# Optimization experiments

Hardware: AMD Instinct MI355X
Metric: run time of the kernel (lower is better)

## Reference

```python
import jax, jax.numpy as jnp
import numpy as np

H = 32  # hidden_size from LSTMConfig

def setup_inputs() -> dict:
    key = jax.random.key(0)
    ks = jax.random.split(key, 7)
    B, T, F = 131072, 22, 12
    s = 1.0 / np.sqrt(H)
    return {
        "x": jax.random.normal(ks[0], (B, T, F), dtype=jnp.float32),
        "W_ih": jax.random.uniform(ks[1], (4 * H, F), minval=-s, maxval=s, dtype=jnp.float32),
        "W_hh": jax.random.uniform(ks[2], (4 * H, H), minval=-s, maxval=s, dtype=jnp.float32),
        "b_ih": jax.random.uniform(ks[3], (4 * H,), minval=-s, maxval=s, dtype=jnp.float32),
        "b_hh": jax.random.uniform(ks[4], (4 * H,), minval=-s, maxval=s, dtype=jnp.float32),
        "W_head": jax.random.uniform(ks[5], (1, H), minval=-s, maxval=s, dtype=jnp.float32),
        "b_head": jax.random.uniform(ks[6], (1,), minval=-s, maxval=s, dtype=jnp.float32),
    }

def _lstm_last_hidden(x, W_ih, W_hh, b_ih, b_hh):
    B, T, F = x.shape
    # precompute input contribution for all timesteps: [T, B, 4H]
    gx = jnp.einsum('btf,gf->tbg', x, W_ih) + (b_ih + b_hh)

    def step(carry, gx_t):
        h, c = carry
        g = gx_t + h @ W_hh.T                      # [B, 4H]
        i, f, gg, o = jnp.split(g, 4, axis=-1)     # PyTorch gate order i,f,g,o
        i = jax.nn.sigmoid(i)
        f = jax.nn.sigmoid(f)
        gg = jnp.tanh(gg)
        o = jax.nn.sigmoid(o)
        c = f * c + i * gg
        h = o * jnp.tanh(c)
        return (h, c), None

    h0 = jnp.zeros((B, H), dtype=x.dtype)
    (h, _), _ = jax.lax.scan(step, (h0, h0), gx)
    return h  # [B, H] last timestep hidden

def reference(x, W_ih, W_hh, b_ih, b_hh, W_head, b_head):
    h = _lstm_last_hidden(x, W_ih, W_hh, b_ih, b_hh)
    # Dropout p=0.0 is identity; Linear(H,1) + Softplus, then squeeze(-1)
    y = h @ W_head.T + b_head                      # [B, 1]
    return jax.nn.softplus(y)[:, 0]                # [B]
```

## Files before the change

### kernel.cpp

```cpp
#include <hip/hip_runtime.h>
#include <math.h>

#define T_STEPS 22
#define F_IN    12
#define HID     32

typedef __attribute__((ext_vector_type(8))) short  bf16x8;
typedef __attribute__((ext_vector_type(16))) float f32x16;

union FragU { unsigned int u[4]; bf16x8 v; };

#define LOG2E    1.442695041f
#define TWOLOG2E 2.885390082f

static __device__ __forceinline__ unsigned short f2bf(float x) {
    unsigned int u = __builtin_bit_cast(unsigned int, x);
    return (unsigned short)((u + 0x7fffu + ((u >> 16) & 1u)) >> 16);
}

static __device__ __forceinline__ unsigned cvt_pk_bf16(float lo, float hi) {
    unsigned r;
    asm("v_cvt_pk_bf16_f32 %0, %1, %2" : "=v"(r) : "v"(lo), "v"(hi));
    return r;
}

__global__ void prep_kernel(const float* __restrict__ Wih, const float* __restrict__ Whh,
                            const float* __restrict__ bih, const float* __restrict__ bhh,
                            const float* __restrict__ Whead, float* __restrict__ ws) {
    const int tid = threadIdx.x;
    unsigned short* wx = (unsigned short*)ws;
    unsigned short* wh = (unsigned short*)(ws + 1024);
    float* whd = ws + 3072;

    {
        int m = tid >> 6, lane = tid & 63;
        int g = 32 * m + (lane & 31);
        float scale = (m == 2) ? TWOLOG2E : -LOG2E;
        int kbase = 8 * (lane >> 5);
        for (int j = 0; j < 8; ++j) {
            int k = kbase + j;
            float v = 0.0f;
            if (k < F_IN)       v = Wih[g * F_IN + k];
            else if (k == F_IN) v = bih[g] + bhh[g];
            wx[tid * 8 + j] = f2bf(scale * v);
        }
    }
    for (int e = tid; e < 4 * 2 * 64; e += 256) {
        int m = e >> 7, kt = (e >> 6) & 1, lane = e & 63;
        int g = 32 * m + (lane & 31);
        float scale = (m == 2) ? TWOLOG2E : -LOG2E;
        int kbase = 16 * kt + 8 * (lane >> 5);
        for (int j = 0; j < 8; ++j)
            wh[e * 8 + j] = f2bf(scale * Whh[g * HID + kbase + j]);
    }
    if (tid < 32) {
        int hi = tid >> 4, q = tid & 15;
        int j = (q & 3) + 8 * (q >> 2) + 4 * hi;
        whd[tid] = Whead[j];
    }
}

__global__ void __launch_bounds__(256, 2)
lstm_kernel(const float* __restrict__ x, const float* __restrict__ ws,
            const float* __restrict__ bheadp, float* __restrict__ out, int B) {
    const int lane = threadIdx.x & 63;
    const int wave = threadIdx.x >> 6;
    const int col  = lane & 31;
    const int hi   = lane >> 5;
    int b = blockIdx.x * 128 + wave * 32 + col;
    const bool valid = (b < B);
    if (b >= B) b = B - 1;

    const bf16x8* wxp = (const bf16x8*)ws;
    const bf16x8* whp = (const bf16x8*)(ws + 1024);
    bf16x8 wxf[4], whf[4][2];
#pragma unroll
    for (int m = 0; m < 4; ++m) wxf[m] = wxp[m * 64 + lane];
#pragma unroll
    for (int m = 0; m < 4; ++m)
#pragma unroll
        for (int kt = 0; kt < 2; ++kt) whf[m][kt] = whp[(m * 2 + kt) * 64 + lane];

    const float* xb1 = x + (size_t)b * (T_STEPS * F_IN) + (hi ? 8 : 0);
    const float* xb2 = x + (size_t)b * (T_STEPS * F_IN) + (hi ? 8 : 4);

    float c[16], hv[16];
#pragma unroll
    for (int q = 0; q < 16; ++q) { c[q] = 0.0f; hv[q] = 0.0f; }
    bf16x8 hf0, hf1;
#pragma unroll
    for (int j = 0; j < 8; ++j) { hf0[j] = 0; hf1[j] = 0; }

    for (int t = 0; t < T_STEPS; ++t) {
        float4 va = *(const float4*)(xb1 + t * F_IN);
        float4 vb = *(const float4*)(xb2 + t * F_IN);

        FragU xf;
        xf.u[0] = cvt_pk_bf16(va.x, va.y);
        xf.u[1] = cvt_pk_bf16(va.z, va.w);
        unsigned w2 = cvt_pk_bf16(vb.x, vb.y);
        unsigned w3 = cvt_pk_bf16(vb.z, vb.w);
        xf.u[2] = hi ? 0x00003f80u : w2;
        xf.u[3] = hi ? 0u : w3;

        f32x16 a0, a1, a2, a3;
#pragma unroll
        for (int q = 0; q < 16; ++q) { a0[q] = 0.f; a1[q] = 0.f; a2[q] = 0.f; a3[q] = 0.f; }

        a0 = __builtin_amdgcn_mfma_f32_32x32x16_bf16(wxf[0], xf.v, a0, 0, 0, 0);
        a1 = __builtin_amdgcn_mfma_f32_32x32x16_bf16(wxf[1], xf.v, a1, 0, 0, 0);
        a2 = __builtin_amdgcn_mfma_f32_32x32x16_bf16(wxf[2], xf.v, a2, 0, 0, 0);
        a3 = __builtin_amdgcn_mfma_f32_32x32x16_bf16(wxf[3], xf.v, a3, 0, 0, 0);
        a0 = __builtin_amdgcn_mfma_f32_32x32x16_bf16(whf[0][0], hf0, a0, 0, 0, 0);
        a1 = __builtin_amdgcn_mfma_f32_32x32x16_bf16(whf[1][0], hf0, a1, 0, 0, 0);
        a2 = __builtin_amdgcn_mfma_f32_32x32x16_bf16(whf[2][0], hf0, a2, 0, 0, 0);
        a3 = __builtin_amdgcn_mfma_f32_32x32x16_bf16(whf[3][0], hf0, a3, 0, 0, 0);
        a0 = __builtin_amdgcn_mfma_f32_32x32x16_bf16(whf[0][1], hf1, a0, 0, 0, 0);
        a1 = __builtin_amdgcn_mfma_f32_32x32x16_bf16(whf[1][1], hf1, a1, 0, 0, 0);
        a2 = __builtin_amdgcn_mfma_f32_32x32x16_bf16(whf[2][1], hf1, a2, 0, 0, 0);
        a3 = __builtin_amdgcn_mfma_f32_32x32x16_bf16(whf[3][1], hf1, a3, 0, 0, 0);

#pragma unroll
        for (int q = 0; q < 16; ++q) {
            float ri = __builtin_amdgcn_rcpf(1.0f + __builtin_amdgcn_exp2f(a0[q]));
            float rf = __builtin_amdgcn_rcpf(1.0f + __builtin_amdgcn_exp2f(a1[q]));
            float rg = __builtin_amdgcn_rcpf(1.0f + __builtin_amdgcn_exp2f(a2[q]));
            float ro = __builtin_amdgcn_rcpf(1.0f + __builtin_amdgcn_exp2f(a3[q]));
            float gs = fmaf(-2.0f * TWOLOG2E, rg, TWOLOG2E);
            c[q] = fmaf(rf, c[q], ri * gs);
            float tc = fmaf(-2.0f, __builtin_amdgcn_rcpf(1.0f + __builtin_amdgcn_exp2f(c[q])), 1.0f);
            hv[q] = ro * tc;
        }

        unsigned P0 = cvt_pk_bf16(hv[0],  hv[1]);
        unsigned P1 = cvt_pk_bf16(hv[2],  hv[3]);
        unsigned P2 = cvt_pk_bf16(hv[4],  hv[5]);
        unsigned P3 = cvt_pk_bf16(hv[6],  hv[7]);
        unsigned P4 = cvt_pk_bf16(hv[8],  hv[9]);
        unsigned P5 = cvt_pk_bf16(hv[10], hv[11]);
        unsigned P6 = cvt_pk_bf16(hv[12], hv[13]);
        unsigned P7 = cvt_pk_bf16(hv[14], hv[15]);
        asm("v_permlane32_swap_b32 %0, %1" : "+v"(P0), "+v"(P2));
        asm("v_permlane32_swap_b32 %0, %1" : "+v"(P1), "+v"(P3));
        asm("v_permlane32_swap_b32 %0, %1" : "+v"(P4), "+v"(P6));
        asm("v_permlane32_swap_b32 %0, %1" : "+v"(P5), "+v"(P7));
        FragU h0; h0.u[0] = P0; h0.u[1] = P1; h0.u[2] = P2; h0.u[3] = P3;
        FragU h1; h1.u[0] = P4; h1.u[1] = P5; h1.u[2] = P6; h1.u[3] = P7;
        hf0 = h0.v;
        hf1 = h1.v;
    }

    const float* whd = ws + 3072 + hi * 16;
    float y = 0.0f;
#pragma unroll
    for (int q = 0; q < 16; ++q) y = fmaf(hv[q], whd[q], y);
    y += __shfl_xor(y, 32, 64);
    y += bheadp[0];
    float sp = fmaxf(y, 0.0f) + log1pf(expf(-fabsf(y)));
    if (valid && hi == 0) out[b] = sp;
}

extern "C" void kernel_launch(void* const* d_in, const int* in_sizes, int n_in,
                              void* d_out, int out_size, void* d_ws, size_t ws_size,
                              hipStream_t stream) {
    const float* x     = (const float*)d_in[0];
    const float* Wih   = (const float*)d_in[1];
    const float* Whh   = (const float*)d_in[2];
    const float* bih   = (const float*)d_in[3];
    const float* bhh   = (const float*)d_in[4];
    const float* Whead = (const float*)d_in[5];
    const float* bhead = (const float*)d_in[6];
    float* out = (float*)d_out;
    float* ws  = (float*)d_ws;

    const int B = in_sizes[0] / (T_STEPS * F_IN);
    const int blocks = (B + 127) / 128;

    hipLaunchKernelGGL(prep_kernel, dim3(1), dim3(256), 0, stream,
                       Wih, Whh, bih, bhh, Whead, ws);
    hipLaunchKernelGGL(lstm_kernel, dim3(blocks), dim3(256), 0, stream,
                       x, ws, bhead, out, B);
}
```

Baseline: 96.32 us.

## Stage LSTM weight fragments in LDS and cut register pressure in recurrence

```diff
diff --git a/kernel.cpp b/kernel.cpp
--- a/kernel.cpp
+++ b/kernel.cpp
@@ -22,6 +22,10 @@
     unsigned r;
     asm("v_cvt_pk_bf16_f32 %0, %1, %2" : "=v"(r) : "v"(lo), "v"(hi));
     return r;
+}
+
+static __device__ __forceinline__ float bf2f(short s) {
+    return __builtin_bit_cast(float, ((unsigned)(unsigned short)s) << 16);
 }
 
 __global__ void prep_kernel(const float* __restrict__ Wih, const float* __restrict__ Whh,
@@ -54,47 +58,49 @@
             wh[e * 8 + j] = f2bf(scale * Whh[g * HID + kbase + j]);
     }
     if (tid < 32) {
-        int hi = tid >> 4, q = tid & 15;
-        int j = (q & 3) + 8 * (q >> 2) + 4 * hi;
-        whd[tid] = Whead[j];
+        int h2 = tid >> 4, j = tid & 15;
+        int k = (j < 8) ? (8 * h2 + j) : (16 + 8 * h2 + (j - 8));
+        whd[tid] = Whead[k];
     }
 }
 
 __global__ void __launch_bounds__(256, 2)
 lstm_kernel(const float* __restrict__ x, const float* __restrict__ ws,
             const float* __restrict__ bheadp, float* __restrict__ out, int B) {
-    const int lane = threadIdx.x & 63;
-    const int wave = threadIdx.x >> 6;
+    const int tid  = threadIdx.x;
+    const int lane = tid & 63;
+    const int wave = tid >> 6;
     const int col  = lane & 31;
     const int hi   = lane >> 5;
     int b = blockIdx.x * 128 + wave * 32 + col;
     const bool valid = (b < B);
     if (b >= B) b = B - 1;
 
-    const bf16x8* wxp = (const bf16x8*)ws;
-    const bf16x8* whp = (const bf16x8*)(ws + 1024);
-    bf16x8 wxf[4], whf[4][2];
-#pragma unroll
-    for (int m = 0; m < 4; ++m) wxf[m] = wxp[m * 64 + lane];
-#pragma unroll
-    for (int m = 0; m < 4; ++m)
-#pragma unroll
-        for (int kt = 0; kt < 2; ++kt) whf[m][kt] = whp[(m * 2 + kt) * 64 + lane];
+    __shared__ float wlds[3072];
+#pragma unroll
+    for (int i = 0; i < 3; ++i)
+        ((float4*)wlds)[tid + i * 256] = ((const float4*)ws)[tid + i * 256];
+    __syncthreads();
+
+    const bf16x8* wx_l = (const bf16x8*)wlds;
+    const bf16x8* wh_l = ((const bf16x8*)wlds) + 256;
 
     const float* xb1 = x + (size_t)b * (T_STEPS * F_IN) + (hi ? 8 : 0);
     const float* xb2 = x + (size_t)b * (T_STEPS * F_IN) + (hi ? 8 : 4);
 
-    float c[16], hv[16];
-#pragma unroll
-    for (int q = 0; q < 16; ++q) { c[q] = 0.0f; hv[q] = 0.0f; }
+    float c[16];
+#pragma unroll
+    for (int q = 0; q < 16; ++q) c[q] = 0.0f;
     bf16x8 hf0, hf1;
 #pragma unroll
     for (int j = 0; j < 8; ++j) { hf0[j] = 0; hf1[j] = 0; }
 
+#pragma unroll 1
     for (int t = 0; t < T_STEPS; ++t) {
+        asm volatile("" ::: "memory");
+
         float4 va = *(const float4*)(xb1 + t * F_IN);
         float4 vb = *(const float4*)(xb2 + t * F_IN);
-
         FragU xf;
         xf.u[0] = cvt_pk_bf16(va.x, va.y);
         xf.u[1] = cvt_pk_bf16(va.z, va.w);
@@ -107,45 +113,56 @@
 #pragma unroll
         for (int q = 0; q < 16; ++q) { a0[q] = 0.f; a1[q] = 0.f; a2[q] = 0.f; a3[q] = 0.f; }
 
-        a0 = __builtin_amdgcn_mfma_f32_32x32x16_bf16(wxf[0], xf.v, a0, 0, 0, 0);
-        a1 = __builtin_amdgcn_mfma_f32_32x32x16_bf16(wxf[1], xf.v, a1, 0, 0, 0);
-        a2 = __builtin_amdgcn_mfma_f32_32x32x16_bf16(wxf[2], xf.v, a2, 0, 0, 0);
-        a3 = __builtin_amdgcn_mfma_f32_32x32x16_bf16(wxf[3], xf.v, a3, 0, 0, 0);
-        a0 = __builtin_amdgcn_mfma_f32_32x32x16_bf16(whf[0][0], hf0, a0, 0, 0, 0);
-        a1 = __builtin_amdgcn_mfma_f32_32x32x16_bf16(whf[1][0], hf0, a1, 0, 0, 0);
-        a2 = __builtin_amdgcn_mfma_f32_32x32x16_bf16(whf[2][0], hf0, a2, 0, 0, 0);
-        a3 = __builtin_amdgcn_mfma_f32_32x32x16_bf16(whf[3][0], hf0, a3, 0, 0, 0);
-        a0 = __builtin_amdgcn_mfma_f32_32x32x16_bf16(whf[0][1], hf1, a0, 0, 0, 0);
-        a1 = __builtin_amdgcn_mfma_f32_32x32x16_bf16(whf[1][1], hf1, a1, 0, 0, 0);
-        a2 = __builtin_amdgcn_mfma_f32_32x32x16_bf16(whf[2][1], hf1, a2, 0, 0, 0);
-        a3 = __builtin_amdgcn_mfma_f32_32x32x16_bf16(whf[3][1], hf1, a3, 0, 0, 0);
-
-#pragma unroll
-        for (int q = 0; q < 16; ++q) {
-            float ri = __builtin_amdgcn_rcpf(1.0f + __builtin_amdgcn_exp2f(a0[q]));
-            float rf = __builtin_amdgcn_rcpf(1.0f + __builtin_amdgcn_exp2f(a1[q]));
-            float rg = __builtin_amdgcn_rcpf(1.0f + __builtin_amdgcn_exp2f(a2[q]));
-            float ro = __builtin_amdgcn_rcpf(1.0f + __builtin_amdgcn_exp2f(a3[q]));
-            float gs = fmaf(-2.0f * TWOLOG2E, rg, TWOLOG2E);
-            c[q] = fmaf(rf, c[q], ri * gs);
-            float tc = fmaf(-2.0f, __builtin_amdgcn_rcpf(1.0f + __builtin_amdgcn_exp2f(c[q])), 1.0f);
-            hv[q] = ro * tc;
+        a0 = __builtin_amdgcn_mfma_f32_32x32x16_bf16(wx_l[0 * 64 + lane], xf.v, a0, 0, 0, 0);
+        a1 = __builtin_amdgcn_mfma_f32_32x32x16_bf16(wx_l[1 * 64 + lane], xf.v, a1, 0, 0, 0);
+        a2 = __builtin_amdgcn_mfma_f32_32x32x16_bf16(wx_l[2 * 64 + lane], xf.v, a2, 0, 0, 0);
+        a3 = __builtin_amdgcn_mfma_f32_32x32x16_bf16(wx_l[3 * 64 + lane], xf.v, a3, 0, 0, 0);
+        a0 = __builtin_amdgcn_mfma_f32_32x32x16_bf16(wh_l[(0 * 2 + 0) * 64 + lane], hf0, a0, 0, 0, 0);
+        a1 = __builtin_amdgcn_mfma_f32_32x32x16_bf16(wh_l[(1 * 2 + 0) * 64 + lane], hf0, a1, 0, 0, 0);
+        a2 = __builtin_amdgcn_mfma_f32_32x32x16_bf16(wh_l[(2 * 2 + 0) * 64 + lane], hf0, a2, 0, 0, 0);
+        a3 = __builtin_amdgcn_mfma_f32_32x32x16_bf16(wh_l[(3 * 2 + 0) * 64 + lane], hf0, a3, 0, 0, 0);
+        a0 = __builtin_amdgcn_mfma_f32_32x32x16_bf16(wh_l[(0 * 2 + 1) * 64 + lane], hf1, a0, 0, 0, 0);
+        a1 = __builtin_amdgcn_mfma_f32_32x32x16_bf16(wh_l[(1 * 2 + 1) * 64 + lane], hf1, a1, 0, 0, 0);
+        a2 = __builtin_amdgcn_mfma_f32_32x32x16_bf16(wh_l[(2 * 2 + 1) * 64 + lane], hf1, a2, 0, 0, 0);
+        a3 = __builtin_amdgcn_mfma_f32_32x32x16_bf16(wh_l[(3 * 2 + 1) * 64 + lane], hf1, a3, 0, 0, 0);
+        __builtin_amdgcn_sched_group_barrier(0x100, 4, 0);
+        __builtin_amdgcn_sched_group_barrier(0x008, 4, 0);
+        __builtin_amdgcn_sched_group_barrier(0x100, 4, 0);
+        __builtin_amdgcn_sched_group_barrier(0x008, 4, 0);
+        __builtin_amdgcn_sched_group_barrier(0x100, 4, 0);
+        __builtin_amdgcn_sched_group_barrier(0x008, 4, 0);
+
+        unsigned P[8];
+#pragma unroll
+        for (int p = 0; p < 8; ++p) {
+            const int q0 = 2 * p, q1 = 2 * p + 1;
+            float ri0 = __builtin_amdgcn_rcpf(1.0f + __builtin_amdgcn_exp2f(a0[q0]));
+            float rf0 = __builtin_amdgcn_rcpf(1.0f + __builtin_amdgcn_exp2f(a1[q0]));
+            float rg0 = __builtin_amdgcn_rcpf(1.0f + __builtin_amdgcn_exp2f(a2[q0]));
+            float ro0 = __builtin_amdgcn_rcpf(1.0f + __builtin_amdgcn_exp2f(a3[q0]));
+            float gs0 = fmaf(-2.0f * TWOLOG2E, rg0, TWOLOG2E);
+            c[q0] = fmaf(rf0, c[q0], ri0 * gs0);
+            float tc0 = fmaf(-2.0f, __builtin_amdgcn_rcpf(1.0f + __builtin_amdgcn_exp2f(c[q0])), 1.0f);
+            float hv0 = ro0 * tc0;
+
+            float ri1 = __builtin_amdgcn_rcpf(1.0f + __builtin_amdgcn_exp2f(a0[q1]));
+            float rf1 = __builtin_amdgcn_rcpf(1.0f + __builtin_amdgcn_exp2f(a1[q1]));
+            float rg1 = __builtin_amdgcn_rcpf(1.0f + __builtin_amdgcn_exp2f(a2[q1]));
+            float ro1 = __builtin_amdgcn_rcpf(1.0f + __builtin_amdgcn_exp2f(a3[q1]));
+            float gs1 = fmaf(-2.0f * TWOLOG2E, rg1, TWOLOG2E);
+            c[q1] = fmaf(rf1, c[q1], ri1 * gs1);
+            float tc1 = fmaf(-2.0f, __builtin_amdgcn_rcpf(1.0f + __builtin_amdgcn_exp2f(c[q1])), 1.0f);
+            float hv1 = ro1 * tc1;
+
+            P[p] = cvt_pk_bf16(hv0, hv1);
         }
 
-        unsigned P0 = cvt_pk_bf16(hv[0],  hv[1]);
-        unsigned P1 = cvt_pk_bf16(hv[2],  hv[3]);
-        unsigned P2 = cvt_pk_bf16(hv[4],  hv[5]);
-        unsigned P3 = cvt_pk_bf16(hv[6],  hv[7]);
-        unsigned P4 = cvt_pk_bf16(hv[8],  hv[9]);
-        unsigned P5 = cvt_pk_bf16(hv[10], hv[11]);
-        unsigned P6 = cvt_pk_bf16(hv[12], hv[13]);
-        unsigned P7 = cvt_pk_bf16(hv[14], hv[15]);
-        asm("v_permlane32_swap_b32 %0, %1" : "+v"(P0), "+v"(P2));
-        asm("v_permlane32_swap_b32 %0, %1" : "+v"(P1), "+v"(P3));
-        asm("v_permlane32_swap_b32 %0, %1" : "+v"(P4), "+v"(P6));
-        asm("v_permlane32_swap_b32 %0, %1" : "+v"(P5), "+v"(P7));
-        FragU h0; h0.u[0] = P0; h0.u[1] = P1; h0.u[2] = P2; h0.u[3] = P3;
-        FragU h1; h1.u[0] = P4; h1.u[1] = P5; h1.u[2] = P6; h1.u[3] = P7;
+        asm("v_permlane32_swap_b32 %0, %1" : "+v"(P[0]), "+v"(P[2]));
+        asm("v_permlane32_swap_b32 %0, %1" : "+v"(P[1]), "+v"(P[3]));
+        asm("v_permlane32_swap_b32 %0, %1" : "+v"(P[4]), "+v"(P[6]));
+        asm("v_permlane32_swap_b32 %0, %1" : "+v"(P[5]), "+v"(P[7]));
+        FragU h0; h0.u[0] = P[0]; h0.u[1] = P[1]; h0.u[2] = P[2]; h0.u[3] = P[3];
+        FragU h1; h1.u[0] = P[4]; h1.u[1] = P[5]; h1.u[2] = P[6]; h1.u[3] = P[7];
         hf0 = h0.v;
         hf1 = h1.v;
     }
@@ -153,7 +170,10 @@
     const float* whd = ws + 3072 + hi * 16;
     float y = 0.0f;
 #pragma unroll
-    for (int q = 0; q < 16; ++q) y = fmaf(hv[q], whd[q], y);
+    for (int j = 0; j < 8; ++j) {
+        y = fmaf(bf2f(hf0[j]), whd[j], y);
+        y = fmaf(bf2f(hf1[j]), whd[8 + j], y);
+    }
     y += __shfl_xor(y, 32, 64);
     y += bheadp[0];
     float sp = fmaxf(y, 0.0f) + log1pf(expf(-fabsf(y)));
```

Measured after the change: 97.43 us. Within noise of the previous version (+1.2%).

## Switch LSTM recurrence to 16x16x32 MFMA tiles with LDS-resident weights

Applied to the files above, without the earlier changes.

```diff
diff --git a/kernel.cpp b/kernel.cpp
--- a/kernel.cpp
+++ b/kernel.cpp
@@ -6,7 +6,7 @@
 #define HID     32
 
 typedef __attribute__((ext_vector_type(8))) short  bf16x8;
-typedef __attribute__((ext_vector_type(16))) float f32x16;
+typedef __attribute__((ext_vector_type(4)))  float f32x4;
 
 union FragU { unsigned int u[4]; bf16x8 v; };
 
@@ -29,135 +29,156 @@
                             const float* __restrict__ Whead, float* __restrict__ ws) {
     const int tid = threadIdx.x;
     unsigned short* wx = (unsigned short*)ws;
-    unsigned short* wh = (unsigned short*)(ws + 1024);
-    float* whd = ws + 3072;
-
-    {
-        int m = tid >> 6, lane = tid & 63;
-        int g = 32 * m + (lane & 31);
-        float scale = (m == 2) ? TWOLOG2E : -LOG2E;
-        int kbase = 8 * (lane >> 5);
+    unsigned short* wh = (unsigned short*)(ws + 2048);
+    float* whd = ws + 4096;
+
+    for (int e = tid; e < 512; e += 256) {
+        int tile = e >> 6, lane = e & 63;
+        int row = lane & 15, s = lane >> 4;
+        int g = 16 * tile + row;
+        float scale = (tile == 4 || tile == 5) ? TWOLOG2E : -LOG2E;
         for (int j = 0; j < 8; ++j) {
-            int k = kbase + j;
+            int k = 8 * s + j;
             float v = 0.0f;
             if (k < F_IN)       v = Wih[g * F_IN + k];
             else if (k == F_IN) v = bih[g] + bhh[g];
-            wx[tid * 8 + j] = f2bf(scale * v);
+            wx[e * 8 + j] = f2bf(scale * v);
+            int cc = (j < 4) ? (4 * s + j) : (16 + 4 * s + (j - 4));
+            wh[e * 8 + j] = f2bf(scale * Whh[g * HID + cc]);
         }
     }
-    for (int e = tid; e < 4 * 2 * 64; e += 256) {
-        int m = e >> 7, kt = (e >> 6) & 1, lane = e & 63;
-        int g = 32 * m + (lane & 31);
-        float scale = (m == 2) ? TWOLOG2E : -LOG2E;
-        int kbase = 16 * kt + 8 * (lane >> 5);
-        for (int j = 0; j < 8; ++j)
-            wh[e * 8 + j] = f2bf(scale * Whh[g * HID + kbase + j]);
-    }
     if (tid < 32) {
-        int hi = tid >> 4, q = tid & 15;
-        int j = (q & 3) + 8 * (q >> 2) + 4 * hi;
-        whd[tid] = Whead[j];
+        int s = tid >> 3, j = tid & 7;
+        int orig = (j < 4) ? (4 * s + j) : (16 + 4 * s + (j - 4));
+        whd[tid] = Whead[orig];
     }
 }
 
 __global__ void __launch_bounds__(256, 2)
 lstm_kernel(const float* __restrict__ x, const float* __restrict__ ws,
             const float* __restrict__ bheadp, float* __restrict__ out, int B) {
-    const int lane = threadIdx.x & 63;
-    const int wave = threadIdx.x >> 6;
-    const int col  = lane & 31;
-    const int hi   = lane >> 5;
-    int b = blockIdx.x * 128 + wave * 32 + col;
+    const int tid  = threadIdx.x;
+    const int lane = tid & 63;
+    const int wave = tid >> 6;
+    const int col  = lane & 15;
+    const int s    = lane >> 4;
+    int b = blockIdx.x * 64 + wave * 16 + col;
     const bool valid = (b < B);
     if (b >= B) b = B - 1;
 
-    const bf16x8* wxp = (const bf16x8*)ws;
-    const bf16x8* whp = (const bf16x8*)(ws + 1024);
-    bf16x8 wxf[4], whf[4][2];
-#pragma unroll
-    for (int m = 0; m < 4; ++m) wxf[m] = wxp[m * 64 + lane];
-#pragma unroll
-    for (int m = 0; m < 4; ++m)
-#pragma unroll
-        for (int kt = 0; kt < 2; ++kt) whf[m][kt] = whp[(m * 2 + kt) * 64 + lane];
-
-    const float* xb1 = x + (size_t)b * (T_STEPS * F_IN) + (hi ? 8 : 0);
-    const float* xb2 = x + (size_t)b * (T_STEPS * F_IN) + (hi ? 8 : 4);
-
-    float c[16], hv[16];
-#pragma unroll
-    for (int q = 0; q < 16; ++q) { c[q] = 0.0f; hv[q] = 0.0f; }
-    bf16x8 hf0, hf1;
-#pragma unroll
-    for (int j = 0; j < 8; ++j) { hf0[j] = 0; hf1[j] = 0; }
-
+    __shared__ float wlds[4096];
+#pragma unroll
+    for (int i = 0; i < 4; ++i)
+        ((float4*)wlds)[tid + i * 256] = ((const float4*)ws)[tid + i * 256];
+    __syncthreads();
+
+    const bf16x8* wx_l = (const bf16x8*)wlds;
+    const bf16x8* wh_l = ((const bf16x8*)wlds) + 512;
+
+    const float* xr  = x + (size_t)b * (T_STEPS * F_IN);
+    const float* xa  = xr + ((s == 0) ? 0 : 8);
+    const float* xbp = xr + ((s == 0) ? 4 : 8);
+
+    float c0[4], c1[4], h0[4], h1[4];
+#pragma unroll
+    for (int q = 0; q < 4; ++q) { c0[q] = 0.f; c1[q] = 0.f; h0[q] = 0.f; h1[q] = 0.f; }
+    bf16x8 hf;
+#pragma unroll
+    for (int j = 0; j < 8; ++j) hf[j] = 0;
+
+    f32x4 zc;
+#pragma unroll
+    for (int q = 0; q < 4; ++q) zc[q] = 0.0f;
+
+#pragma unroll 1
     for (int t = 0; t < T_STEPS; ++t) {
-        float4 va = *(const float4*)(xb1 + t * F_IN);
-        float4 vb = *(const float4*)(xb2 + t * F_IN);
-
+        asm volatile("" ::: "memory");
+
+        float4 va = *(const float4*)(xa  + t * F_IN);
+        float4 vb = *(const float4*)(xbp + t * F_IN);
+        unsigned p0 = cvt_pk_bf16(va.x, va.y);
+        unsigned p1 = cvt_pk_bf16(va.z, va.w);
+        unsigned p2 = cvt_pk_bf16(vb.x, vb.y);
+        unsigned p3 = cvt_pk_bf16(vb.z, vb.w);
         FragU xf;
-        xf.u[0] = cvt_pk_bf16(va.x, va.y);
-        xf.u[1] = cvt_pk_bf16(va.z, va.w);
-        unsigned w2 = cvt_pk_bf16(vb.x, vb.y);
-        unsigned w3 = cvt_pk_bf16(vb.z, vb.w);
-        xf.u[2] = hi ? 0x00003f80u : w2;
-        xf.u[3] = hi ? 0u : w3;
-
-        f32x16 a0, a1, a2, a3;
-#pragma unroll
-        for (int q = 0; q < 16; ++q) { a0[q] = 0.f; a1[q] = 0.f; a2[q] = 0.f; a3[q] = 0.f; }
-
-        a0 = __builtin_amdgcn_mfma_f32_32x32x16_bf16(wxf[0], xf.v, a0, 0, 0, 0);
-        a1 = __builtin_amdgcn_mfma_f32_32x32x16_bf16(wxf[1], xf.v, a1, 0, 0, 0);
-        a2 = __builtin_amdgcn_mfma_f32_32x32x16_bf16(wxf[2], xf.v, a2, 0, 0, 0);
-        a3 = __builtin_amdgcn_mfma_f32_32x32x16_bf16(wxf[3], xf.v, a3, 0, 0, 0);
-        a0 = __builtin_amdgcn_mfma_f32_32x32x16_bf16(whf[0][0], hf0, a0, 0, 0, 0);
-        a1 = __builtin_amdgcn_mfma_f32_32x32x16_bf16(whf[1][0], hf0, a1, 0, 0, 0);
-        a2 = __builtin_amdgcn_mfma_f32_32x32x16_bf16(whf[2][0], hf0, a2, 0, 0, 0);
-        a3 = __builtin_amdgcn_mfma_f32_32x32x16_bf16(whf[3][0], hf0, a3, 0, 0, 0);
-        a0 = __builtin_amdgcn_mfma_f32_32x32x16_bf16(whf[0][1], hf1, a0, 0, 0, 0);
-        a1 = __builtin_amdgcn_mfma_f32_32x32x16_bf16(whf[1][1], hf1, a1, 0, 0, 0);
-        a2 = __builtin_amdgcn_mfma_f32_32x32x16_bf16(whf[2][1], hf1, a2, 0, 0, 0);
-        a3 = __builtin_amdgcn_mfma_f32_32x32x16_bf16(whf[3][1], hf1, a3, 0, 0, 0);
-
-#pragma unroll
-        for (int q = 0; q < 16; ++q) {
+        if (s == 0)      { xf.u[0] = p0; xf.u[1] = p1; xf.u[2] = p2;          xf.u[3] = p3; }
+        else if (s == 1) { xf.u[0] = p0; xf.u[1] = p1; xf.u[2] = 0x00003f80u; xf.u[3] = 0;  }
+        else             { xf.u[0] = 0;  xf.u[1] = 0;  xf.u[2] = 0;           xf.u[3] = 0;  }
+
+        f32x4 a0, a1, a2, a3, a4, a5, a6, a7;
+        a0 = __builtin_amdgcn_mfma_f32_16x16x32_bf16(wx_l[0 * 64 + lane], xf.v, zc, 0, 0, 0);
+        a1 = __builtin_amdgcn_mfma_f32_16x16x32_bf16(wx_l[1 * 64 + lane], xf.v, zc, 0, 0, 0);
+        a2 = __builtin_amdgcn_mfma_f32_16x16x32_bf16(wx_l[2 * 64 + lane], xf.v, zc, 0, 0, 0);
+        a3 = __builtin_amdgcn_mfma_f32_16x16x32_bf16(wx_l[3 * 64 + lane], xf.v, zc, 0, 0, 0);
+        a4 = __builtin_amdgcn_mfma_f32_16x16x32_bf16(wx_l[4 * 64 + lane], xf.v, zc, 0, 0, 0);
+        a5 = __builtin_amdgcn_mfma_f32_16x16x32_bf16(wx_l[5 * 64 + lane], xf.v, zc, 0, 0, 0);
+        a6 = __builtin_amdgcn_mfma_f32_16x16x32_bf16(wx_l[6 * 64 + lane], xf.v, zc, 0, 0, 0);
+        a7 = __builtin_amdgcn_mfma_f32_16x16x32_bf16(wx_l[7 * 64 + lane], xf.v, zc, 0, 0, 0);
+        a0 = __builtin_amdgcn_mfma_f32_16x16x32_bf16(wh_l[0 * 64 + lane], hf, a0, 0, 0, 0);
+        a1 = __builtin_amdgcn_mfma_f32_16x16x32_bf16(wh_l[1 * 64 + lane], hf, a1, 0, 0, 0);
+        a2 = __builtin_amdgcn_mfma_f32_16x16x32_bf16(wh_l[2 * 64 + lane], hf, a2, 0, 0, 0);
+        a3 = __builtin_amdgcn_mfma_f32_16x16x32_bf16(wh_l[3 * 64 + lane], hf, a3, 0, 0, 0);
+        a4 = __builtin_amdgcn_mfma_f32_16x16x32_bf16(wh_l[4 * 64 + lane], hf, a4, 0, 0, 0);
+        a5 = __builtin_amdgcn_mfma_f32_16x16x32_bf16(wh_l[5 * 64 + lane], hf, a5, 0, 0, 0);
+        a6 = __builtin_amdgcn_mfma_f32_16x16x32_bf16(wh_l[6 * 64 + lane], hf, a6, 0, 0, 0);
+        a7 = __builtin_amdgcn_mfma_f32_16x16x32_bf16(wh_l[7 * 64 + lane], hf, a7, 0, 0, 0);
+        __builtin_amdgcn_sched_group_barrier(0x100, 2, 0);
+        __builtin_amdgcn_sched_group_barrier(0x008, 2, 0);
+        __builtin_amdgcn_sched_group_barrier(0x100, 2, 0);
+        __builtin_amdgcn_sched_group_barrier(0x008, 2, 0);
+        __builtin_amdgcn_sched_group_barrier(0x100, 2, 0);
+        __builtin_amdgcn_sched_group_barrier(0x008, 2, 0);
+        __builtin_amdgcn_sched_group_barrier(0x100, 2, 0);
+        __builtin_amdgcn_sched_group_barrier(0x008, 2, 0);
+        __builtin_amdgcn_sched_group_barrier(0x100, 2, 0);
+        __builtin_amdgcn_sched_group_barrier(0x008, 2, 0);
+        __builtin_amdgcn_sched_group_barrier(0x100, 2, 0);
+        __builtin_amdgcn_sched_group_barrier(0x008, 2, 0);
+        __builtin_amdgcn_sched_group_barrier(0x100, 2, 0);
+        __builtin_amdgcn_sched_group_barrier(0x008, 2, 0);
+        __builtin_amdgcn_sched_group_barrier(0x100, 2, 0);
+        __builtin_amdgcn_sched_group_barrier(0x008, 2, 0);
+
+#pragma unroll
+        for (int q = 0; q < 4; ++q) {
             float ri = __builtin_amdgcn_rcpf(1.0f + __builtin_amdgcn_exp2f(a0[q]));
-            float rf = __builtin_amdgcn_rcpf(1.0f + __builtin_amdgcn_exp2f(a1[q]));
-            float rg = __builtin_amdgcn_rcpf(1.0f + __builtin_amdgcn_exp2f(a2[q]));
-            float ro = __builtin_amdgcn_rcpf(1.0f + __builtin_amdgcn_exp2f(a3[q]));
+            float rf = __builtin_amdgcn_rcpf(1.0f + __builtin_amdgcn_exp2f(a2[q]));
+            float rg = __builtin_amdgcn_rcpf(1.0f + __builtin_amdgcn_exp2f(a4[q]));
+            float ro = __builtin_amdgcn_rcpf(1.0f + __builtin_amdgcn_exp2f(a6[q]));
             float gs = fmaf(-2.0f * TWOLOG2E, rg, TWOLOG2E);
-            c[q] = fmaf(rf, c[q], ri * gs);
-            float tc = fmaf(-2.0f, __builtin_amdgcn_rcpf(1.0f + __builtin_amdgcn_exp2f(c[q])), 1.0f);
-            hv[q] = ro * tc;
+            c0[q] = fmaf(rf, c0[q], ri * gs);
+            float tc = fmaf(-2.0f, __builtin_amdgcn_rcpf(1.0f + __builtin_amdgcn_exp2f(c0[q])), 1.0f);
+            h0[q] = ro * tc;
+            float si = __builtin_amdgcn_rcpf(1.0f + __builtin_amdgcn_exp2f(a1[q]));
+            float sf = __builtin_amdgcn_rcpf(1.0f + __builtin_amdgcn_exp2f(a3[q]));
+            float sg = __builtin_amdgcn_rcpf(1.0f + __builtin_amdgcn_exp2f(a5[q]));
+            float so = __builtin_amdgcn_rcpf(1.0f + __builtin_amdgcn_exp2f(a7[q]));
+            float gt = fmaf(-2.0f * TWOLOG2E, sg, TWOLOG2E);
+            c1[q] = fmaf(sf, c1[q], si * gt);
+            float td = fmaf(-2.0f, __builtin_amdgcn_rcpf(1.0f + __builtin_amdgcn_exp2f(c1[q])), 1.0f);
+            h1[q] = so * td;
         }
 
-        unsigned P0 = cvt_pk_bf16(hv[0],  hv[1]);
-        unsigned P1 = cvt_pk_bf16(hv[2],  hv[3]);
-        unsigned P2 = cvt_pk_bf16(hv[4],  hv[5]);
-        unsigned P3 = cvt_pk_bf16(hv[6],  hv[7]);
-        unsigned P4 = cvt_pk_bf16(hv[8],  hv[9]);
-        unsigned P5 = cvt_pk_bf16(hv[10], hv[11]);
-        unsigned P6 = cvt_pk_bf16(hv[12], hv[13]);
-        unsigned P7 = cvt_pk_bf16(hv[14], hv[15]);
-        asm("v_permlane32_swap_b32 %0, %1" : "+v"(P0), "+v"(P2));
-        asm("v_permlane32_swap_b32 %0, %1" : "+v"(P1), "+v"(P3));
-        asm("v_permlane32_swap_b32 %0, %1" : "+v"(P4), "+v"(P6));
-        asm("v_permlane32_swap_b32 %0, %1" : "+v"(P5), "+v"(P7));
-        FragU h0; h0.u[0] = P0; h0.u[1] = P1; h0.u[2] = P2; h0.u[3] = P3;
-        FragU h1; h1.u[0] = P4; h1.u[1] = P5; h1.u[2] = P6; h1.u[3] = P7;
-        hf0 = h0.v;
-        hf1 = h1.v;
-    }
-
-    const float* whd = ws + 3072 + hi * 16;
+        FragU hh;
+        hh.u[0] = cvt_pk_bf16(h0[0], h0[1]);
+        hh.u[1] = cvt_pk_bf16(h0[2], h0[3]);
+        hh.u[2] = cvt_pk_bf16(h1[0], h1[1]);
+        hh.u[3] = cvt_pk_bf16(h1[2], h1[3]);
+        hf = hh.v;
+    }
+
+    const float* whd = ws + 4096 + s * 8;
     float y = 0.0f;
 #pragma unroll
-    for (int q = 0; q < 16; ++q) y = fmaf(hv[q], whd[q], y);
+    for (int j = 0; j < 4; ++j) {
+        y = fmaf(h0[j], whd[j],     y);
+        y = fmaf(h1[j], whd[4 + j], y);
+    }
+    y += __shfl_xor(y, 16, 64);
     y += __shfl_xor(y, 32, 64);
     y += bheadp[0];
     float sp = fmaxf(y, 0.0f) + log1pf(expf(-fabsf(y)));
-    if (valid && hi == 0) out[b] = sp;
+    if (valid && s == 0) out[b] = sp;
 }
 
 extern "C" void kernel_launch(void* const* d_in, const int* in_sizes, int n_in,
@@ -174,7 +195,7 @@
     float* ws  = (float*)d_ws;
 
     const int B = in_sizes[0] / (T_STEPS * F_IN);
-    const int blocks = (B + 127) / 128;
+    const int blocks = (B + 63) / 64;
 
     hipLaunchKernelGGL(prep_kernel, dim3(1), dim3(256), 0, stream,
                        Wih, Whh, bih, bhh, Whead, ws);
```

Result: slower. 111.5 us (+15.8%).
